# Performance work log

Hardware: AMD Instinct MI355X
Metric: run time of the kernel (lower is better)

Reference implementation:

```python
import jax, jax.numpy as jnp
import numpy as np

N_NODES = 100000
N_EDGES = 1600000
FEAT = 32
HID = 32
N_GRAPHS = 64


def setup_inputs() -> dict:
    key = jax.random.key(0)
    ks = jax.random.split(key, 12)
    x = jax.random.normal(ks[0], (N_NODES, FEAT), dtype=jnp.float32)
    edge_index = jax.random.randint(ks[1], (2, N_EDGES), 0, N_NODES, dtype=jnp.int64)
    batch = jnp.sort(jax.random.randint(ks[2], (N_NODES,), 0, N_GRAPHS, dtype=jnp.int64))
    # ChebConv (K=3) params: one linear per Chebyshev order + shared bias
    W_cheb = jax.random.normal(ks[3], (3, FEAT, HID), dtype=jnp.float32) * 0.1
    b_cheb = jnp.zeros((HID,), dtype=jnp.float32)
    # MLP head 32 -> 1024 -> 512 -> 4
    W1 = jax.random.normal(ks[4], (HID, 1024), dtype=jnp.float32) * 0.05
    b1 = jnp.zeros((1024,), dtype=jnp.float32)
    W2 = jax.random.normal(ks[5], (1024, 512), dtype=jnp.float32) * 0.05
    b2 = jnp.zeros((512,), dtype=jnp.float32)
    W3 = jax.random.normal(ks[6], (512, 4), dtype=jnp.float32) * 0.05
    b3 = jnp.zeros((4,), dtype=jnp.float32)
    return {"x": x, "edge_index": edge_index, "batch": batch,
            "W_cheb": W_cheb, "b_cheb": b_cheb,
            "W1": W1, "b1": b1, "W2": W2, "b2": b2, "W3": W3, "b3": b3}


def reference(x, edge_index, batch, W_cheb, b_cheb, W1, b1, W2, b2, W3, b3):
    row, col = edge_index[0], edge_index[1]  # source, target
    n = x.shape[0]
    # symmetric normalization of scaled Laplacian (lambda_max=2, no self loops):
    # L_hat = -D^{-1/2} A D^{-1/2}
    deg = jax.ops.segment_sum(jnp.ones((row.shape[0],), x.dtype), row, num_segments=n)
    dis = jnp.where(deg > 0, jax.lax.rsqrt(jnp.where(deg > 0, deg, 1.0)), 0.0)
    norm = -(dis[row] * dis[col])  # [E]

    def prop(h):  # L_hat @ h via gather -> scale -> scatter-add
        return jax.ops.segment_sum(norm[:, None] * h[row], col, num_segments=n)

    # Chebyshev recursion: T0=x, T1=L_hat x, T2=2 L_hat T1 - T0
    Tx0 = x
    Tx1 = prop(Tx0)
    Tx2 = 2.0 * prop(Tx1) - Tx0
    h = Tx0 @ W_cheb[0] + Tx1 @ W_cheb[1] + Tx2 @ W_cheb[2] + b_cheb  # [N, HID]
    # global max pool per graph
    g = jax.ops.segment_max(h, batch, num_segments=N_GRAPHS)  # [B, HID]
    # MLP head (dropout/LeakyReLU defined but unused in original forward)
    h1 = jax.nn.relu(g @ W1 + b1)
    h2 = jax.nn.relu(h1 @ W2 + b2)
    return h2 @ W3 + b3  # [B, 4]
```

## Files before the change

kernel.cpp:

```cpp
#include <hip/hip_runtime.h>
#include <hip/hip_fp16.h>


#define NT 256
#define NTS 1024
#define BSHIFT 8
#define BSIZE 256
#define HB 256
#define CAPC 48
#define CAPR 64
#define CAP 5120

typedef _Float16 half8 __attribute__((ext_vector_type(8)));
typedef float f32x4 __attribute__((ext_vector_type(4)));

__device__ __forceinline__ void atomicMaxFloat(float* addr, float val) {
    if (val >= 0.0f) atomicMax((int*)addr, __float_as_int(val));
    else             atomicMin((unsigned int*)addr, __float_as_uint(val));
}

#define ACC8(raw)                                        \
    do {                                                 \
        const __half2* hp_ = (const __half2*)&(raw);     \
        float2 f0_ = __half22float2(hp_[0]);             \
        float2 f1_ = __half22float2(hp_[1]);             \
        float2 f2_ = __half22float2(hp_[2]);             \
        float2 f3_ = __half22float2(hp_[3]);             \
        a0 += f0_.x; a1 += f0_.y; a2 += f1_.x; a3 += f1_.y; \
        a4 += f2_.x; a5 += f2_.y; a6 += f3_.x; a7 += f3_.y; \
    } while (0)

__global__ __launch_bounds__(512) void k_init(float* __restrict__ g,
                                              const float* __restrict__ Wc,
                                              _Float16* __restrict__ wfrag,
                                              int* __restrict__ bcur,
                                              int* __restrict__ rcur, int NBK) {
    int tid = threadIdx.x;
    for (int i = tid; i < 64 * 32; i += 512) g[i] = -__builtin_inff();
    if (tid < 384) {
        int combo = tid >> 6, lane = tid & 63;
        int mat = combo >> 1, n = combo & 1;
        int m = lane & 15, quad = lane >> 4;
        #pragma unroll
        for (int j = 0; j < 8; j++)
            wfrag[(size_t)combo * 512 + lane * 8 + j] =
                (_Float16)Wc[mat * 1024 + (quad * 8 + j) * 32 + n * 16 + m];
    }
    if (tid < NBK) {
        bcur[tid] = tid * CAP;
        rcur[tid] = tid * CAP;
    }
}

__global__ __launch_bounds__(NTS) void k_bscatter(const int* __restrict__ row,
                                                  const int* __restrict__ col,
                                                  int* __restrict__ bcur,
                                                  int* __restrict__ rcur,
                                                  int* __restrict__ ebuck,
                                                  unsigned char* __restrict__ rbuck,
                                                  int E, int NBK, int epb) {
    __shared__ int cntc[512], cntr[512];
    __shared__ int basec[512], baser[512];
    __shared__ int cstage[512 * CAPC];
    __shared__ unsigned char rstage[512 * CAPR];
    int tid = threadIdx.x;
    if (tid < 512) { cntc[tid] = 0; cntr[tid] = 0; }
    __syncthreads();
    int start = blockIdx.x * epb;
    int end = min(start + epb, E);
    for (int e = start + tid; e < end; e += NTS) {
        int r = row[e], c = col[e];
        int bc_ = c >> BSHIFT;
        int li = atomicAdd(&cntc[bc_], 1);
        if (li < CAPC)
            cstage[bc_ * CAPC + li] = (r << BSHIFT) | (c & (BSIZE - 1));
        int br_ = r >> BSHIFT;
        int lj = atomicAdd(&cntr[br_], 1);
        if (lj < CAPR)
            rstage[br_ * CAPR + lj] = (unsigned char)(r & (BSIZE - 1));
    }
    __syncthreads();
    if (tid < 512) {
        int n = min(cntc[tid], CAPC);
        basec[tid] = n ? atomicAdd(&bcur[tid], n) : 0;
    } else {
        int b = tid - 512;
        int n = min(cntr[b], CAPR);
        baser[b] = n ? atomicAdd(&rcur[b], n) : 0;
    }
    __syncthreads();
    int warp = tid >> 6, lane = tid & 63;
    for (int b = warp; b < NBK; b += (NTS >> 6)) {
        int n = min(cntc[b], CAPC);
        int base = basec[b];
        for (int i = lane; i < n; i += 64)
            ebuck[base + i] = cstage[b * CAPC + i];
    }
    for (int b = warp; b < NBK; b += (NTS >> 6)) {
        int n = min(cntr[b], CAPR);
        int base = baser[b];
        for (int i = lane; i < n; i += 64)
            rbuck[base + i] = rstage[b * CAPR + i];
    }
}

__global__ __launch_bounds__(NT) void k_prep(
    const int* __restrict__ rcur, const unsigned char* __restrict__ rbuck,
    const int* __restrict__ bcur, const int* __restrict__ ebuck,
    const float* __restrict__ x,
    float* __restrict__ dis, float* __restrict__ rdis,
    __half* __restrict__ xh, __half* __restrict__ xsh,
    int* __restrict__ offs, int* __restrict__ entries, int N) {
    __shared__ int cnt[1024];
    __shared__ int tsum[256];
    __shared__ float sdis[256];
    int b = blockIdx.x, tid = threadIdx.x;
    int rbase = b * CAP, rend = rcur[b];
    int ebase = b * CAP, eend = bcur[b];
    cnt[tid] = 0; cnt[tid + 256] = 0; cnt[tid + 512] = 0; cnt[tid + 768] = 0;
    __syncthreads();
    for (int e = rbase + tid; e < rend; e += NT)
        atomicAdd(&cnt[rbuck[e]], 1);
    __syncthreads();
    int dcount = cnt[tid];
    int node = (b << BSHIFT) + tid;
    float d = (dcount > 0) ? rsqrtf((float)dcount) : 0.0f;
    if (node < N) {
        dis[node] = d;
        rdis[node] = (dcount > 0) ? sqrtf((float)dcount) : 0.0f;
    }
    sdis[tid] = d;
    __syncthreads();
    cnt[tid] = 0; cnt[tid + 256] = 0; cnt[tid + 512] = 0; cnt[tid + 768] = 0;
    __syncthreads();
    for (int e = ebase + tid; e < eend; e += NT) {
        int pv = ebuck[e];
        atomicAdd(&cnt[((pv & (BSIZE - 1)) << 2) | ((pv >> BSHIFT) >> 15)], 1);
    }
    __syncthreads();
    int s0 = cnt[tid * 4], s1 = cnt[tid * 4 + 1], s2 = cnt[tid * 4 + 2], s3 = cnt[tid * 4 + 3];
    int tot = s0 + s1 + s2 + s3;
    tsum[tid] = tot;
    __syncthreads();
    for (int off = 1; off < 256; off <<= 1) {
        int t = (tid >= off) ? tsum[tid - off] : 0;
        __syncthreads();
        tsum[tid] += t;
        __syncthreads();
    }
    int excl = tsum[tid] - tot;
    if (node < N) offs[node] = ((ebase + excl) << 9) | tot;
    cnt[tid * 4]     = ebase + excl;
    cnt[tid * 4 + 1] = ebase + excl + s0;
    cnt[tid * 4 + 2] = ebase + excl + s0 + s1;
    cnt[tid * 4 + 3] = ebase + excl + s0 + s1 + s2;
    __syncthreads();
    for (int e = ebase + tid; e < eend; e += NT) {
        int pv = ebuck[e];
        int src = pv >> BSHIFT;
        int li = atomicAdd(&cnt[((pv & (BSIZE - 1)) << 2) | (src >> 15)], 1);
        entries[li] = src;
    }
    int nodebase = b << BSHIFT;
    for (int i4 = tid; i4 < 2048; i4 += NT) {
        int gnode = nodebase + (i4 >> 3);
        if (gnode >= N) break;
        float4 v = ((const float4*)x)[(size_t)nodebase * 8 + i4];
        float dd = sdis[i4 >> 3];
        float2 o, os;
        ((__half2*)&o)[0] = __floats2half2_rn(v.x, v.y);
        ((__half2*)&o)[1] = __floats2half2_rn(v.z, v.w);
        ((__half2*)&os)[0] = __floats2half2_rn(dd * v.x, dd * v.y);
        ((__half2*)&os)[1] = __floats2half2_rn(dd * v.z, dd * v.w);
        ((float2*)xh)[(size_t)nodebase * 8 + i4] = o;
        ((float2*)xsh)[(size_t)nodebase * 8 + i4] = os;
    }
}

__global__ __launch_bounds__(NT) void k_prop1(const int* __restrict__ offs,
                                              const int* __restrict__ entries,
                                              const float* __restrict__ dis,
                                              const __half* __restrict__ xsh,
                                              __half* __restrict__ xs2h, int N) {
    int idx = blockIdx.x * blockDim.x + threadIdx.x;
    int node = idx >> 3, sp = (idx >> 2) & 1, q = idx & 3;
    if (node >= N) return;
    int pv = offs[node];
    int s = pv >> 9, deg = pv & 511;
    int mid = s + (deg >> 1), t = s + deg;
    int lo = sp ? mid : s;
    int hi = sp ? t : mid;
    float a0 = 0, a1 = 0, a2 = 0, a3 = 0, a4 = 0, a5 = 0, a6 = 0, a7 = 0;
    for (int e = lo; e < hi; e++) {
        int r = entries[e];
        float4 w = *(const float4*)(xsh + (size_t)r * 32 + q * 8);
        ACC8(w);
    }
    a0 += __shfl_xor(a0, 4); a1 += __shfl_xor(a1, 4);
    a2 += __shfl_xor(a2, 4); a3 += __shfl_xor(a3, 4);
    a4 += __shfl_xor(a4, 4); a5 += __shfl_xor(a5, 4);
    a6 += __shfl_xor(a6, 4); a7 += __shfl_xor(a7, 4);
    if (sp == 0) {
        float d = dis[node];
        float sd = -d * d;
        float4 ov;
        ((__half2*)&ov)[0] = __floats2half2_rn(sd * a0, sd * a1);
        ((__half2*)&ov)[1] = __floats2half2_rn(sd * a2, sd * a3);
        ((__half2*)&ov)[2] = __floats2half2_rn(sd * a4, sd * a5);
        ((__half2*)&ov)[3] = __floats2half2_rn(sd * a6, sd * a7);
        *(float4*)(xs2h + (size_t)node * 32 + q * 8) = ov;
    }
}

__global__ __launch_bounds__(NT) void k_combine_f(
    const int* __restrict__ offs, const int* __restrict__ entries,
    const float* __restrict__ dis, const float* __restrict__ rdis,
    const __half* __restrict__ xs2h, const _Float16* __restrict__ xh,
    const _Float16* __restrict__ wfrag, const float* __restrict__ bc,
    const int* __restrict__ batch, float* __restrict__ g, int N) {
    __shared__ float sb[32];
    __shared__ float sp2[64][33];
    __shared__ float hs[64][33];
    __shared__ int sbatch[64];

    int tid = threadIdx.x;
    if (tid < 32) sb[tid] = bc[tid];
    int rowbase = blockIdx.x * 64;
    if (tid >= 64 && tid < 128) {
        int gr = rowbase + tid - 64;
        sbatch[tid - 64] = (gr < N) ? batch[gr] : -1;
    }

    int node_l = tid >> 2, q = tid & 3;
    int gnode = rowbase + node_l;
    if (gnode < N) {
        int pv = offs[gnode];
        int s = pv >> 9, t = s + (pv & 511);
        float a0 = 0, a1 = 0, a2 = 0, a3 = 0, a4 = 0, a5 = 0, a6 = 0, a7 = 0;
        for (int e = s; e < t; e++) {
            int r = entries[e];
            float4 w = *(const float4*)(xs2h + (size_t)r * 32 + q * 8);
            ACC8(w);
        }
        float sc = -dis[gnode];
        float* p = &sp2[node_l][q * 8];
        p[0] = sc * a0; p[1] = sc * a1; p[2] = sc * a2; p[3] = sc * a3;
        p[4] = sc * a4; p[5] = sc * a5; p[6] = sc * a6; p[7] = sc * a7;
    }
    __syncthreads();

    int wave = tid >> 6;
    int lane = tid & 63;
    int m = lane & 15;
    int quad = lane >> 4;
    int grow = rowbase + wave * 16 + m;

    half8 a0 = {}, a1 = {}, a2 = {};
    if (grow < N) {
        size_t off = (size_t)grow * 32 + quad * 8;
        a0 = *(const half8*)(xh + off);
        half8 x2 = *(const half8*)((const _Float16*)xs2h + off);
        float rd = rdis[grow];
        const float* p = &sp2[wave * 16 + m][quad * 8];
        #pragma unroll
        for (int j = 0; j < 8; j++) {
            a1[j] = (_Float16)((float)x2[j] * rd);
            a2[j] = (_Float16)(2.0f * p[j] - (float)a0[j]);
        }
    }

    const half8* wf = (const half8*)wfrag;
    f32x4 acc[2];
    #pragma unroll
    for (int n = 0; n < 2; n++) {
        f32x4 c = {0.f, 0.f, 0.f, 0.f};
        c = __builtin_amdgcn_mfma_f32_16x16x32_f16(a0, wf[(0 * 2 + n) * 64 + lane], c, 0, 0, 0);
        c = __builtin_amdgcn_mfma_f32_16x16x32_f16(a1, wf[(1 * 2 + n) * 64 + lane], c, 0, 0, 0);
        c = __builtin_amdgcn_mfma_f32_16x16x32_f16(a2, wf[(2 * 2 + n) * 64 + lane], c, 0, 0, 0);
        acc[n] = c;
    }

    #pragma unroll
    for (int n = 0; n < 2; n++)
        #pragma unroll
        for (int r = 0; r < 4; r++)
            hs[wave * 16 + quad * 4 + r][n * 16 + m] = acc[n][r] + sb[n * 16 + m];
    __syncthreads();

    int f = tid & 31, s = tid >> 5;
    int curb = -1;
    float curm = 0.0f;
    for (int j = s * 8; j < s * 8 + 8; j++) {
        int b = sbatch[j];
        if (b < 0) continue;
        float v = hs[j][f];
        if (b != curb) {
            if (curb >= 0) atomicMaxFloat(&g[curb * 32 + f], curm);
            curb = b;
            curm = v;
        } else {
            curm = fmaxf(curm, v);
        }
    }
    if (curb >= 0) atomicMaxFloat(&g[curb * 32 + f], curm);
}

__global__ __launch_bounds__(NT) void k_mlp12(const float* __restrict__ g,
                                              const float* __restrict__ W1,
                                              const float* __restrict__ b1,
                                              const float* __restrict__ W2,
                                              float* __restrict__ h2acc) {
    __shared__ float sg[32];
    __shared__ float sh[128];
    int gi = blockIdx.x >> 3, ks = blockIdx.x & 7;
    int tid = threadIdx.x;
    if (tid < 32) sg[tid] = g[gi * 32 + tid];
    __syncthreads();
    if (tid < 128) {
        int c = ks * 128 + tid;
        float a = b1[c];
        #pragma unroll
        for (int k = 0; k < 32; k++) a += sg[k] * W1[k * 1024 + c];
        sh[tid] = fmaxf(a, 0.0f);
    }
    __syncthreads();
    const float* w = W2 + (size_t)(ks * 128) * 512;
    float acc0 = 0.0f, acc1 = 0.0f;
    for (int k = 0; k < 128; k++) {
        float h = sh[k];
        acc0 += h * w[k * 512 + tid];
        acc1 += h * w[k * 512 + tid + 256];
    }
    atomicAdd(&h2acc[gi * 512 + tid], acc0);
    atomicAdd(&h2acc[gi * 512 + tid + 256], acc1);
}

__global__ __launch_bounds__(NT) void k_mlp3p(const float* __restrict__ h2acc,
                                              const float* __restrict__ b2,
                                              const float* __restrict__ W3,
                                              const float* __restrict__ b3,
                                              float* __restrict__ out) {
    __shared__ float sp[256];
    int gi = blockIdx.x;
    int tid = threadIdx.x;
    int j = tid & 3, slot = tid >> 2;
    float part = 0.0f;
    #pragma unroll
    for (int kk = 0; kk < 8; kk++) {
        int k = slot * 8 + kk;
        float h = fmaxf(h2acc[gi * 512 + k] + b2[k], 0.0f);
        part += h * W3[k * 4 + j];
    }
    sp[tid] = part;
    __syncthreads();
    for (int s = 32; s >= 1; s >>= 1) {
        if (slot < s) sp[tid] += sp[(slot + s) * 4 + j];
        __syncthreads();
    }
    if (slot == 0) out[gi * 4 + j] = sp[j] + b3[j];
}

extern "C" void kernel_launch(void* const* d_in, const int* in_sizes, int n_in,
                              void* d_out, int out_size, void* d_ws, size_t ws_size,
                              hipStream_t stream) {
    const float* x   = (const float*)d_in[0];
    const int* ei    = (const int*)d_in[1];
    const int* batch = (const int*)d_in[2];
    const float* Wc  = (const float*)d_in[3];
    const float* bc  = (const float*)d_in[4];
    const float* W1  = (const float*)d_in[5];
    const float* b1  = (const float*)d_in[6];
    const float* W2  = (const float*)d_in[7];
    const float* b2  = (const float*)d_in[8];
    const float* W3  = (const float*)d_in[9];
    const float* b3  = (const float*)d_in[10];
    float* out       = (float*)d_out;

    const int N = in_sizes[2];
    const int E = in_sizes[1] / 2;
    const int* row = ei;
    const int* col = ei + E;
    const int NBK = (N + BSIZE - 1) / BSIZE;
    const int epb = (E + HB - 1) / HB;
    const size_t PADE = (size_t)NBK * CAP;

    float* h2acc    = (float*)d_ws;
    int* bcur       = (int*)(h2acc + 64 * 512);
    int* rcur       = bcur + 512;
    float* dis      = (float*)(rcur + 512);
    float* rdis     = dis + N;
    int* offs       = (int*)(rdis + N);
    int* ebuck      = offs + N + 4;
    unsigned char* rbuck = (unsigned char*)(ebuck + PADE);
    int* entries    = (int*)(rbuck + PADE);
    _Float16* xh    = (_Float16*)(entries + PADE);
    _Float16* xsh   = xh + (size_t)N * 32;
    _Float16* xs2h  = xsh + (size_t)N * 32;
    float* g        = (float*)(xs2h + (size_t)N * 32);
    _Float16* wfrag = (_Float16*)(g + 64 * 32);

    hipMemsetAsync(h2acc, 0, sizeof(float) * 64 * 512, stream);

    k_init<<<1, 512, 0, stream>>>(g, Wc, wfrag, bcur, rcur, NBK);
    k_bscatter<<<HB, NTS, 0, stream>>>(row, col, bcur, rcur, ebuck, rbuck, E, NBK, epb);
    k_prep<<<NBK, NT, 0, stream>>>(rcur, rbuck, bcur, ebuck, x, dis, rdis,
                                   (__half*)xh, (__half*)xsh, offs, entries, N);
    k_prop1<<<((size_t)N * 8 + NT - 1) / NT, NT, 0, stream>>>(offs, entries, dis, (const __half*)xsh, (__half*)xs2h, N);
    k_combine_f<<<(N + 63) / 64, NT, 0, stream>>>(offs, entries, dis, rdis, (const __half*)xs2h, xh, wfrag, bc, batch, g, N);
    k_mlp12<<<512, NT, 0, stream>>>(g, W1, b1, W2, h2acc);
    k_mlp3p<<<64, NT, 0, stream>>>(h2acc, b2, W3, b3, out);
}
```

Baseline: 210.3 us.

## Unroll gather loops, pre-reduce pool max in LDS, drop MLP atomics and memset

The neighbour-gather loops in the propagation and combine kernels are unrolled by four so several independent row loads are in flight at once. Global max-pooling now reduces into a shared-memory table per block before issuing one global atomic per graph-feature, which cuts global atomic traffic. The MLP layer-2 partial sums are written to a per-split buffer and summed in the final kernel, so the float atomicAdds and the memset are no longer needed. The costs are more registers in the gather loops and extra shared memory in the combine kernel.

```diff
diff --git a/kernel.cpp b/kernel.cpp
--- a/kernel.cpp
+++ b/kernel.cpp
@@ -191,7 +191,16 @@
     int lo = sp ? mid : s;
     int hi = sp ? t : mid;
     float a0 = 0, a1 = 0, a2 = 0, a3 = 0, a4 = 0, a5 = 0, a6 = 0, a7 = 0;
-    for (int e = lo; e < hi; e++) {
+    int e = lo;
+    for (; e + 4 <= hi; e += 4) {
+        int r0 = entries[e], r1 = entries[e + 1], r2 = entries[e + 2], r3 = entries[e + 3];
+        float4 w0 = *(const float4*)(xsh + (size_t)r0 * 32 + q * 8);
+        float4 w1 = *(const float4*)(xsh + (size_t)r1 * 32 + q * 8);
+        float4 w2 = *(const float4*)(xsh + (size_t)r2 * 32 + q * 8);
+        float4 w3 = *(const float4*)(xsh + (size_t)r3 * 32 + q * 8);
+        ACC8(w0); ACC8(w1); ACC8(w2); ACC8(w3);
+    }
+    for (; e < hi; e++) {
         int r = entries[e];
         float4 w = *(const float4*)(xsh + (size_t)r * 32 + q * 8);
         ACC8(w);
@@ -221,7 +230,9 @@
     __shared__ float sb[32];
     __shared__ float sp2[64][33];
     __shared__ float hs[64][33];
+    __shared__ float lmax[64][32];
     __shared__ int sbatch[64];
+    __shared__ int s_blo, s_bhi;
 
     int tid = threadIdx.x;
     if (tid < 32) sb[tid] = bc[tid];
@@ -237,7 +248,16 @@
         int pv = offs[gnode];
         int s = pv >> 9, t = s + (pv & 511);
         float a0 = 0, a1 = 0, a2 = 0, a3 = 0, a4 = 0, a5 = 0, a6 = 0, a7 = 0;
-        for (int e = s; e < t; e++) {
+        int e = s;
+        for (; e + 4 <= t; e += 4) {
+            int r0 = entries[e], r1 = entries[e + 1], r2 = entries[e + 2], r3 = entries[e + 3];
+            float4 w0 = *(const float4*)(xs2h + (size_t)r0 * 32 + q * 8);
+            float4 w1 = *(const float4*)(xs2h + (size_t)r1 * 32 + q * 8);
+            float4 w2 = *(const float4*)(xs2h + (size_t)r2 * 32 + q * 8);
+            float4 w3 = *(const float4*)(xs2h + (size_t)r3 * 32 + q * 8);
+            ACC8(w0); ACC8(w1); ACC8(w2); ACC8(w3);
+        }
+        for (; e < t; e++) {
             int r = entries[e];
             float4 w = *(const float4*)(xs2h + (size_t)r * 32 + q * 8);
             ACC8(w);
@@ -285,31 +305,47 @@
         #pragma unroll
         for (int r = 0; r < 4; r++)
             hs[wave * 16 + quad * 4 + r][n * 16 + m] = acc[n][r] + sb[n * 16 + m];
-    __syncthreads();
-
-    int f = tid & 31, s = tid >> 5;
+    if (tid == 0) {
+        int lo = sbatch[0];
+        int hi = lo;
+        for (int j = 63; j > 0; j--) {
+            if (sbatch[j] >= 0) { hi = sbatch[j]; break; }
+        }
+        s_blo = lo; s_bhi = hi;
+    }
+    __syncthreads();
+
+    int bspan = s_bhi - s_blo + 1;
+    for (int i = tid; i < bspan * 32; i += NT) lmax[i >> 5][i & 31] = -__builtin_inff();
+    __syncthreads();
+    int f = tid & 31, sg = tid >> 5;
     int curb = -1;
     float curm = 0.0f;
-    for (int j = s * 8; j < s * 8 + 8; j++) {
+    for (int j = sg * 8; j < sg * 8 + 8; j++) {
         int b = sbatch[j];
         if (b < 0) continue;
         float v = hs[j][f];
         if (b != curb) {
-            if (curb >= 0) atomicMaxFloat(&g[curb * 32 + f], curm);
+            if (curb >= 0) atomicMaxFloat(&lmax[curb - s_blo][f], curm);
             curb = b;
             curm = v;
         } else {
             curm = fmaxf(curm, v);
         }
     }
-    if (curb >= 0) atomicMaxFloat(&g[curb * 32 + f], curm);
+    if (curb >= 0) atomicMaxFloat(&lmax[curb - s_blo][f], curm);
+    __syncthreads();
+    for (int i = tid; i < bspan * 32; i += NT) {
+        float v = lmax[i >> 5][i & 31];
+        if (v > -__builtin_inff()) atomicMaxFloat(&g[(s_blo + (i >> 5)) * 32 + (i & 31)], v);
+    }
 }
 
 __global__ __launch_bounds__(NT) void k_mlp12(const float* __restrict__ g,
                                               const float* __restrict__ W1,
                                               const float* __restrict__ b1,
                                               const float* __restrict__ W2,
-                                              float* __restrict__ h2acc) {
+                                              float* __restrict__ h2part) {
     __shared__ float sg[32];
     __shared__ float sh[128];
     int gi = blockIdx.x >> 3, ks = blockIdx.x & 7;
@@ -331,25 +367,32 @@
         acc0 += h * w[k * 512 + tid];
         acc1 += h * w[k * 512 + tid + 256];
     }
-    atomicAdd(&h2acc[gi * 512 + tid], acc0);
-    atomicAdd(&h2acc[gi * 512 + tid + 256], acc1);
-}
-
-__global__ __launch_bounds__(NT) void k_mlp3p(const float* __restrict__ h2acc,
+    h2part[gi * 4096 + ks * 512 + tid] = acc0;
+    h2part[gi * 4096 + ks * 512 + tid + 256] = acc1;
+}
+
+__global__ __launch_bounds__(NT) void k_mlp3p(const float* __restrict__ h2part,
                                               const float* __restrict__ b2,
                                               const float* __restrict__ W3,
                                               const float* __restrict__ b3,
                                               float* __restrict__ out) {
+    __shared__ float sh2[512];
     __shared__ float sp[256];
     int gi = blockIdx.x;
     int tid = threadIdx.x;
+    for (int k = tid; k < 512; k += NT) {
+        float s = 0.0f;
+        #pragma unroll
+        for (int p = 0; p < 8; p++) s += h2part[gi * 4096 + p * 512 + k];
+        sh2[k] = fmaxf(s + b2[k], 0.0f);
+    }
+    __syncthreads();
     int j = tid & 3, slot = tid >> 2;
     float part = 0.0f;
     #pragma unroll
     for (int kk = 0; kk < 8; kk++) {
         int k = slot * 8 + kk;
-        float h = fmaxf(h2acc[gi * 512 + k] + b2[k], 0.0f);
-        part += h * W3[k * 4 + j];
+        part += sh2[k] * W3[k * 4 + j];
     }
     sp[tid] = part;
     __syncthreads();
@@ -384,8 +427,8 @@
     const int epb = (E + HB - 1) / HB;
     const size_t PADE = (size_t)NBK * CAP;
 
-    float* h2acc    = (float*)d_ws;
-    int* bcur       = (int*)(h2acc + 64 * 512);
+    float* h2part   = (float*)d_ws;
+    int* bcur       = (int*)(h2part + 64 * 4096);
     int* rcur       = bcur + 512;
     float* dis      = (float*)(rcur + 512);
     float* rdis     = dis + N;
@@ -399,14 +442,12 @@
     float* g        = (float*)(xs2h + (size_t)N * 32);
     _Float16* wfrag = (_Float16*)(g + 64 * 32);
 
-    hipMemsetAsync(h2acc, 0, sizeof(float) * 64 * 512, stream);
-
     k_init<<<1, 512, 0, stream>>>(g, Wc, wfrag, bcur, rcur, NBK);
     k_bscatter<<<HB, NTS, 0, stream>>>(row, col, bcur, rcur, ebuck, rbuck, E, NBK, epb);
     k_prep<<<NBK, NT, 0, stream>>>(rcur, rbuck, bcur, ebuck, x, dis, rdis,
                                    (__half*)xh, (__half*)xsh, offs, entries, N);
     k_prop1<<<((size_t)N * 8 + NT - 1) / NT, NT, 0, stream>>>(offs, entries, dis, (const __half*)xsh, (__half*)xs2h, N);
     k_combine_f<<<(N + 63) / 64, NT, 0, stream>>>(offs, entries, dis, rdis, (const __half*)xs2h, xh, wfrag, bc, batch, g, N);
-    k_mlp12<<<512, NT, 0, stream>>>(g, W1, b1, W2, h2acc);
-    k_mlp3p<<<64, NT, 0, stream>>>(h2acc, b2, W3, b3, out);
-}
+    k_mlp12<<<512, NT, 0, stream>>>(g, W1, b1, W2, h2part);
+    k_mlp3p<<<64, NT, 0, stream>>>(h2part, b2, W3, b3, out);
+}
```

Result: faster. 192.2 us (-8.6%).
